# Kernel tuning notes

Hardware: AMD Instinct MI355X
Metric: run time of the kernel (lower is better)

## Reference

```python
import jax, jax.numpy as jnp
import numpy as np

N = 100000
E = 1_600_000
IN_DIM = 128
HIDDEN = 128


def spmm(row, col, vals, H):
    # y[r] = sum_{edges e with row[e]==r} vals[e] * H[col[e]]
    msgs = vals[:, None] * H[col]          # [E, hidden] gather + scale
    return jax.ops.segment_sum(msgs, row, num_segments=H.shape[0])


def setup_inputs() -> dict:
    key = jax.random.key(0)
    ks = jax.random.split(key, 10)
    X = jax.random.normal(ks[0], (N, IN_DIM), dtype=jnp.float32)
    row = jax.random.randint(ks[1], (E,), 0, N, dtype=jnp.int32)
    col = jax.random.randint(ks[2], (E,), 0, N, dtype=jnp.int32)
    vals = jax.random.uniform(ks[3], (E,), dtype=jnp.float32)
    s_in = 1.0 / np.sqrt(IN_DIM)
    s_h = 1.0 / np.sqrt(HIDDEN)
    W_in = jax.random.normal(ks[4], (IN_DIM, HIDDEN), dtype=jnp.float32) * s_in
    b_in = jax.random.normal(ks[5], (HIDDEN,), dtype=jnp.float32) * s_in
    W_mp1 = jax.random.normal(ks[6], (HIDDEN, HIDDEN), dtype=jnp.float32) * s_h
    W_mp2 = jax.random.normal(ks[7], (HIDDEN, HIDDEN), dtype=jnp.float32) * s_h
    W_out = jax.random.normal(ks[8], (HIDDEN, 1), dtype=jnp.float32) * s_h
    b_out = jax.random.normal(ks[9], (1,), dtype=jnp.float32) * s_h
    return {"X": X, "row": row, "col": col, "vals": vals,
            "W_in": W_in, "b_in": b_in, "W_mp1": W_mp1, "W_mp2": W_mp2,
            "W_out": W_out, "b_out": b_out}


def reference(X, row, col, vals, W_in, b_in, W_mp1, W_mp2, W_out, b_out):
    H = jax.nn.relu(X @ W_in + b_in)          # [N, hidden]
    AH = spmm(row, col, vals, H)              # 1-hop propagation
    A2H = spmm(row, col, vals, AH)            # 2-hop propagation
    H2 = jax.nn.relu(AH @ W_mp1 + A2H @ W_mp2)
    return H2 @ W_out + b_out                 # [N, 1]
```

## Files before the change

### kernel.cpp

```cpp
#include <hip/hip_runtime.h>

#define N_NODES 100000
#define N_EDGES 1600000
#define NBUCK 391
#define NCHUNK 256
#define CHUNK 6250
#define LROW 136
#define DCAP 5120

typedef float f32x4 __attribute__((ext_vector_type(4)));
typedef _Float16 f16x8 __attribute__((ext_vector_type(8)));
typedef _Float16 h16x2 __attribute__((ext_vector_type(2)));

__device__ __forceinline__ unsigned f2h_bits(float f) {
    union { _Float16 h; unsigned short s; } c;
    c.h = (_Float16)f;
    return c.s;
}
__device__ __forceinline__ h16x2 u2h(unsigned u) {
    union { unsigned u; h16x2 h; } c;
    c.u = u;
    return c.h;
}
__device__ __forceinline__ unsigned pk16lo(unsigned hi, unsigned lo) {
    return __builtin_amdgcn_perm(hi, lo, 0x05040100u);
}
__device__ __forceinline__ unsigned pk16hi(unsigned hi, unsigned lo) {
    return __builtin_amdgcn_perm(hi, lo, 0x07060302u);
}
__device__ __forceinline__ float fdot2(h16x2 a, h16x2 b, float c) {
#if __has_builtin(__builtin_amdgcn_fdot2)
    return __builtin_amdgcn_fdot2(a, b, c, false);
#else
    return c + (float)a[0] * (float)b[0] + (float)a[1] * (float)b[1];
#endif
}

__device__ __forceinline__ f16x8 pack_h8(float4 a, float4 b) {
    f16x8 r;
    r[0] = (_Float16)a.x; r[1] = (_Float16)a.y;
    r[2] = (_Float16)a.z; r[3] = (_Float16)a.w;
    r[4] = (_Float16)b.x; r[5] = (_Float16)b.y;
    r[6] = (_Float16)b.z; r[7] = (_Float16)b.w;
    return r;
}


__global__ __launch_bounds__(256) void k_prep(const int* __restrict__ row,
                                              int* __restrict__ hmat,
                                              const float* __restrict__ Wa,
                                              const float* __restrict__ Wb,
                                              const float* __restrict__ Wc,
                                              unsigned short* __restrict__ Wta,
                                              unsigned short* __restrict__ Wtb,
                                              unsigned short* __restrict__ Wtc) {
    if (blockIdx.x < NCHUNK) {
        __shared__ int h[NBUCK];
        for (int i = threadIdx.x; i < NBUCK; i += 256) h[i] = 0;
        __syncthreads();
        int s = blockIdx.x * CHUNK, e = s + CHUNK;
        for (int i = s + threadIdx.x; i < e; i += 256)
            atomicAdd(&h[row[i] >> 8], 1);
        __syncthreads();
        for (int b = threadIdx.x; b < NBUCK; b += 256)
            hmat[blockIdx.x * NBUCK + b] = h[b];
    } else {
        int t = (blockIdx.x - NCHUNK) * 256 + threadIdx.x;
        int which = t >> 14;
        int i = t & 16383;
        int n = i & 127, k = i >> 7;
        const float* W = which == 0 ? Wa : which == 1 ? Wb : Wc;
        unsigned short* Wt = which == 0 ? Wta : which == 1 ? Wtb : Wtc;
        Wt[n * 128 + k] = (unsigned short)f2h_bits(W[k * 128 + n]);
    }
}

__global__ __launch_bounds__(512) void k_colscanB(const int* __restrict__ hmat,
                                                  int* __restrict__ bases,
                                                  int* __restrict__ bstart) {
    __shared__ int s[512];
    int b = blockIdx.x, t = threadIdx.x;
    if (b < NBUCK) {
        int v = (t < NCHUNK) ? hmat[t * NBUCK + b] : 0;
        s[t] = v;
        __syncthreads();
        for (int off = 1; off < 512; off <<= 1) {
            int x = (t >= off) ? s[t - off] : 0;
            __syncthreads();
            s[t] += x;
            __syncthreads();
        }
        if (t < NCHUNK) bases[t * NBUCK + b] = s[t] - v;
    } else {
        int v = 0;
        if (t < NBUCK) {
            for (int blk = 0; blk < NCHUNK; blk++) v += hmat[blk * NBUCK + t];
        }
        s[t] = v;
        __syncthreads();
        for (int off = 1; off < 512; off <<= 1) {
            int x = (t >= off) ? s[t - off] : 0;
            __syncthreads();
            s[t] += x;
            __syncthreads();
        }
        if (t < NBUCK) bstart[t] = s[t] - v;
        if (t == NBUCK) bstart[NBUCK] = N_EDGES;
    }
}

__global__ __launch_bounds__(256) void k_binC(const int* __restrict__ row,
                                              const int* __restrict__ col,
                                              const float* __restrict__ vals,
                                              const int* __restrict__ bstart,
                                              const int* __restrict__ bases,
                                              int2* __restrict__ grouped) {
    __shared__ int cnt[NBUCK];
    for (int i = threadIdx.x; i < NBUCK; i += 256) cnt[i] = 0;
    __syncthreads();
    int s = blockIdx.x * CHUNK, e = s + CHUNK;
    for (int i = s + threadIdx.x; i < e; i += 256) {
        int r = row[i];
        int b = r >> 8;
        int rank = atomicAdd(&cnt[b], 1);
        int pos = bstart[b] + bases[blockIdx.x * NBUCK + b] + rank;
        unsigned hv = f2h_bits(vals[i]);
        grouped[pos] = make_int2(col[i], ((r & 255) << 14) | hv);
    }
}

__global__ __launch_bounds__(256) void k_binD(const int2* __restrict__ grouped,
                                              const int* __restrict__ bstart,
                                              unsigned* __restrict__ evf,
                                              int* __restrict__ row_ptr) {
    __shared__ int h[256], sc[256], cur[256];
    __shared__ int2 ebuf[DCAP];
    int b = blockIdx.x, t = threadIdx.x;
    int s0 = bstart[b], e0 = bstart[b + 1];
    int n = e0 - s0;
    bool inlds = (n <= DCAP);
    h[t] = 0;
    __syncthreads();
    if (inlds) {
        for (int i = t; i < n; i += 256) ebuf[i] = grouped[s0 + i];
        __syncthreads();
        for (int i = t; i < n; i += 256)
            atomicAdd(&h[(ebuf[i].y >> 14) & 255], 1);
    } else {
        for (int i = s0 + t; i < e0; i += 256)
            atomicAdd(&h[(grouped[i].y >> 14) & 255], 1);
    }
    __syncthreads();
    int v = h[t];
    sc[t] = v;
    __syncthreads();
    for (int off = 1; off < 256; off <<= 1) {
        int x = (t >= off) ? sc[t - off] : 0;
        __syncthreads();
        sc[t] += x;
        __syncthreads();
    }
    int excl = sc[t] - v;
    cur[t] = excl;
    int grow = b * 256 + t;
    if (grow <= N_NODES) row_ptr[grow] = s0 + excl;
    __syncthreads();
    if (inlds) {
        for (int i = t; i < n; i += 256) {
            int2 g = ebuf[i];
            int rl = (g.y >> 14) & 255;
            int p = atomicAdd(&cur[rl], 1);
            evf[s0 + p] = ((unsigned)g.x << 14) | (unsigned)(g.y & 0x3fff);
        }
    } else {
        for (int i = s0 + t; i < e0; i += 256) {
            int2 g = grouped[i];
            int rl = (g.y >> 14) & 255;
            int p = atomicAdd(&cur[rl], 1);
            evf[s0 + p] = ((unsigned)g.x << 14) | (unsigned)(g.y & 0x3fff);
        }
    }
}

__global__ __launch_bounds__(256) void k_gemm_in(const float* __restrict__ X,
                                                 const unsigned short* __restrict__ Wt,
                                                 const float* __restrict__ b,
                                                 unsigned short* __restrict__ H) {
    __shared__ unsigned short lds[64 * LROW];
    int tid = threadIdx.x;
    int lane = tid & 63, wv = tid >> 6;
    int quad = lane >> 4, c16 = lane & 15;

    f16x8 wf[2][4];
    float bb[2];
#pragma unroll
    for (int nt = 0; nt < 2; nt++) {
        int ng = wv * 2 + nt;
        bb[nt] = b[ng * 16 + c16];
#pragma unroll
        for (int kc = 0; kc < 4; kc++)
            wf[nt][kc] = *(const f16x8*)&Wt[(ng * 16 + c16) * 128 + kc * 32 + quad * 8];
    }

    int tilebase = blockIdx.x * 64;
    const float4* Xg = (const float4*)X;
#pragma unroll
    for (int i = 0; i < 4; i++) {
        int c = tid + i * 256;
        int r = c >> 4, o = c & 15;
        int grow = tilebase + r;
        float4 f0 = make_float4(0.f, 0.f, 0.f, 0.f), f1 = f0;
        if (grow < N_NODES) {
            f0 = Xg[(size_t)grow * 32 + o * 2];
            f1 = Xg[(size_t)grow * 32 + o * 2 + 1];
        }
        *(f16x8*)&lds[r * LROW + o * 8] = pack_h8(f0, f1);
    }
    __syncthreads();

    f32x4 acc[4][2] = {};
#pragma unroll
    for (int t4 = 0; t4 < 4; t4++) {
#pragma unroll
        for (int kc = 0; kc < 4; kc++) {
            f16x8 af = *(const f16x8*)&lds[(t4 * 16 + c16) * LROW + kc * 32 + quad * 8];
#pragma unroll
            for (int nt = 0; nt < 2; nt++)
                acc[t4][nt] = __builtin_amdgcn_mfma_f32_16x16x32_f16(af, wf[nt][kc],
                                                                    acc[t4][nt], 0, 0, 0);
        }
    }
    __syncthreads();

#pragma unroll
    for (int t4 = 0; t4 < 4; t4++)
#pragma unroll
        for (int nt = 0; nt < 2; nt++) {
            int ncol = (wv * 2 + nt) * 16 + c16;
#pragma unroll
            for (int r = 0; r < 4; r++) {
                float v = fmaxf(acc[t4][nt][r] + bb[nt], 0.f);
                lds[(t4 * 16 + quad * 4 + r) * LROW + ncol] = (unsigned short)f2h_bits(v);
            }
        }
    __syncthreads();
#pragma unroll
    for (int i = 0; i < 4; i++) {
        int c = tid + i * 256;
        int r = c >> 4, o = c & 15;
        int grow = tilebase + r;
        if (grow < N_NODES)
            *(uint4*)&H[(size_t)grow * 128 + o * 8] = *(const uint4*)&lds[r * LROW + o * 8];
    }
}

__global__ __launch_bounds__(256) void k_spmm(const int* __restrict__ rp,
                                              const unsigned* __restrict__ evf,
                                              const unsigned* __restrict__ Hin,
                                              unsigned* __restrict__ Ho) {
    int wid = (blockIdx.x * blockDim.x + threadIdx.x) >> 6;
    int lane = threadIdx.x & 63;
    if (wid >= N_NODES) return;
    int q = lane >> 4, l16 = lane & 15;
    int s = __builtin_amdgcn_readfirstlane(rp[wid]);
    int e = __builtin_amdgcn_readfirstlane(rp[wid + 1]);
    float a0 = 0.f, a1 = 0.f, a2 = 0.f, a3 = 0.f;
    float a4 = 0.f, a5 = 0.f, a6 = 0.f, a7 = 0.f;
    for (int base = s; base < e; base += 64) {
        int cnt = e - base;
        if (cnt > 64) cnt = 64;
        unsigned ev = evf[base + (lane < cnt ? lane : cnt - 1)];
        int r = 0;
        for (; r + 16 <= cnt; r += 16) {
            unsigned u0 = __shfl(ev, r + q, 64);
            unsigned u1 = __shfl(ev, r + 4 + q, 64);
            unsigned u2 = __shfl(ev, r + 8 + q, 64);
            unsigned u3 = __shfl(ev, r + 12 + q, 64);
            const uint4 h0 = *(const uint4*)&Hin[(size_t)(u0 >> 14) * 64 + l16 * 4];
            const uint4 h1 = *(const uint4*)&Hin[(size_t)(u1 >> 14) * 64 + l16 * 4];
            const uint4 h2 = *(const uint4*)&Hin[(size_t)(u2 >> 14) * 64 + l16 * 4];
            const uint4 h3 = *(const uint4*)&Hin[(size_t)(u3 >> 14) * 64 + l16 * 4];
            h16x2 v01 = u2h(pk16lo(u1 & 0x3fffu, u0 & 0x3fffu));
            h16x2 v23 = u2h(pk16lo(u3 & 0x3fffu, u2 & 0x3fffu));
            a0 = fdot2(v01, u2h(pk16lo(h1.x, h0.x)), a0);
            a0 = fdot2(v23, u2h(pk16lo(h3.x, h2.x)), a0);
            a1 = fdot2(v01, u2h(pk16hi(h1.x, h0.x)), a1);
            a1 = fdot2(v23, u2h(pk16hi(h3.x, h2.x)), a1);
            a2 = fdot2(v01, u2h(pk16lo(h1.y, h0.y)), a2);
            a2 = fdot2(v23, u2h(pk16lo(h3.y, h2.y)), a2);
            a3 = fdot2(v01, u2h(pk16hi(h1.y, h0.y)), a3);
            a3 = fdot2(v23, u2h(pk16hi(h3.y, h2.y)), a3);
            a4 = fdot2(v01, u2h(pk16lo(h1.z, h0.z)), a4);
            a4 = fdot2(v23, u2h(pk16lo(h3.z, h2.z)), a4);
            a5 = fdot2(v01, u2h(pk16hi(h1.z, h0.z)), a5);
            a5 = fdot2(v23, u2h(pk16hi(h3.z, h2.z)), a5);
            a6 = fdot2(v01, u2h(pk16lo(h1.w, h0.w)), a6);
            a6 = fdot2(v23, u2h(pk16lo(h3.w, h2.w)), a6);
            a7 = fdot2(v01, u2h(pk16hi(h1.w, h0.w)), a7);
            a7 = fdot2(v23, u2h(pk16hi(h3.w, h2.w)), a7);
        }
        if (r < cnt) {
            int i0 = r + q, i1 = r + 4 + q, i2 = r + 8 + q, i3 = r + 12 + q;
            unsigned u0 = __shfl(ev, i0 < cnt ? i0 : cnt - 1, 64);
            unsigned u1 = __shfl(ev, i1 < cnt ? i1 : cnt - 1, 64);
            unsigned u2 = __shfl(ev, i2 < cnt ? i2 : cnt - 1, 64);
            unsigned u3 = __shfl(ev, i3 < cnt ? i3 : cnt - 1, 64);
            const uint4 h0 = *(const uint4*)&Hin[(size_t)(u0 >> 14) * 64 + l16 * 4];
            const uint4 h1 = *(const uint4*)&Hin[(size_t)(u1 >> 14) * 64 + l16 * 4];
            const uint4 h2 = *(const uint4*)&Hin[(size_t)(u2 >> 14) * 64 + l16 * 4];
            const uint4 h3 = *(const uint4*)&Hin[(size_t)(u3 >> 14) * 64 + l16 * 4];
            unsigned m0 = (i0 < cnt) ? (u0 & 0x3fffu) : 0u;
            unsigned m1 = (i1 < cnt) ? (u1 & 0x3fffu) : 0u;
            unsigned m2 = (i2 < cnt) ? (u2 & 0x3fffu) : 0u;
            unsigned m3 = (i3 < cnt) ? (u3 & 0x3fffu) : 0u;
            h16x2 v01 = u2h(pk16lo(m1, m0));
            h16x2 v23 = u2h(pk16lo(m3, m2));
            a0 = fdot2(v01, u2h(pk16lo(h1.x, h0.x)), a0);
            a0 = fdot2(v23, u2h(pk16lo(h3.x, h2.x)), a0);
            a1 = fdot2(v01, u2h(pk16hi(h1.x, h0.x)), a1);
            a1 = fdot2(v23, u2h(pk16hi(h3.x, h2.x)), a1);
            a2 = fdot2(v01, u2h(pk16lo(h1.y, h0.y)), a2);
            a2 = fdot2(v23, u2h(pk16lo(h3.y, h2.y)), a2);
            a3 = fdot2(v01, u2h(pk16hi(h1.y, h0.y)), a3);
            a3 = fdot2(v23, u2h(pk16hi(h3.y, h2.y)), a3);
            a4 = fdot2(v01, u2h(pk16lo(h1.z, h0.z)), a4);
            a4 = fdot2(v23, u2h(pk16lo(h3.z, h2.z)), a4);
            a5 = fdot2(v01, u2h(pk16hi(h1.z, h0.z)), a5);
            a5 = fdot2(v23, u2h(pk16hi(h3.z, h2.z)), a5);
            a6 = fdot2(v01, u2h(pk16lo(h1.w, h0.w)), a6);
            a6 = fdot2(v23, u2h(pk16lo(h3.w, h2.w)), a6);
            a7 = fdot2(v01, u2h(pk16hi(h1.w, h0.w)), a7);
            a7 = fdot2(v23, u2h(pk16hi(h3.w, h2.w)), a7);
        }
    }
    a0 += __shfl_xor(a0, 16, 64); a0 += __shfl_xor(a0, 32, 64);
    a1 += __shfl_xor(a1, 16, 64); a1 += __shfl_xor(a1, 32, 64);
    a2 += __shfl_xor(a2, 16, 64); a2 += __shfl_xor(a2, 32, 64);
    a3 += __shfl_xor(a3, 16, 64); a3 += __shfl_xor(a3, 32, 64);
    a4 += __shfl_xor(a4, 16, 64); a4 += __shfl_xor(a4, 32, 64);
    a5 += __shfl_xor(a5, 16, 64); a5 += __shfl_xor(a5, 32, 64);
    a6 += __shfl_xor(a6, 16, 64); a6 += __shfl_xor(a6, 32, 64);
    a7 += __shfl_xor(a7, 16, 64); a7 += __shfl_xor(a7, 32, 64);
    if (q == 0) {
        uint4 p;
        p.x = (f2h_bits(a1) << 16) | f2h_bits(a0);
        p.y = (f2h_bits(a3) << 16) | f2h_bits(a2);
        p.z = (f2h_bits(a5) << 16) | f2h_bits(a4);
        p.w = (f2h_bits(a7) << 16) | f2h_bits(a6);
        *(uint4*)&Ho[(size_t)wid * 64 + l16 * 4] = p;
    }
}

__global__ __launch_bounds__(256) void k_gemm_out(const unsigned short* __restrict__ AH,
                                                  const unsigned short* __restrict__ A2H,
                                                  const unsigned short* __restrict__ Wt1,
                                                  const unsigned short* __restrict__ Wt2,
                                                  const float* __restrict__ Wout,
                                                  const float* __restrict__ bout,
                                                  float* __restrict__ out) {
    __shared__ unsigned short lds[2][64 * LROW];
    __shared__ float part[4][64];
    int tid = threadIdx.x;
    int lane = tid & 63, wv = tid >> 6;
    int quad = lane >> 4, c16 = lane & 15;

    f16x8 w1f[2][4], w2f[2][4];
    float wo[2];
#pragma unroll
    for (int nt = 0; nt < 2; nt++) {
        int ng = wv * 2 + nt;
        wo[nt] = Wout[ng * 16 + c16];
#pragma unroll
        for (int kc = 0; kc < 4; kc++) {
            w1f[nt][kc] = *(const f16x8*)&Wt1[(ng * 16 + c16) * 128 + kc * 32 + quad * 8];
            w2f[nt][kc] = *(const f16x8*)&Wt2[(ng * 16 + c16) * 128 + kc * 32 + quad * 8];
        }
    }
    float bo = bout[0];

    int tilebase = blockIdx.x * 64;
    const uint4* Ag = (const uint4*)(AH + (size_t)tilebase * 128);
    const uint4* Bg = (const uint4*)(A2H + (size_t)tilebase * 128);
#pragma unroll
    for (int i = 0; i < 4; i++) {
        int c = tid + i * 256;
        int r = c >> 4, o = c & 15;
        *(uint4*)&lds[0][r * LROW + o * 8] = Ag[c];
        *(uint4*)&lds[1][r * LROW + o * 8] = Bg[c];
    }
    __syncthreads();

    f32x4 acc[4][2] = {};
#pragma unroll
    for (int t4 = 0; t4 < 4; t4++) {
#pragma unroll
        for (int kc = 0; kc < 4; kc++) {
            f16x8 afA = *(const f16x8*)&lds[0][(t4 * 16 + c16) * LROW + kc * 32 + quad * 8];
            f16x8 afB = *(const f16x8*)&lds[1][(t4 * 16 + c16) * LROW + kc * 32 + quad * 8];
#pragma unroll
            for (int nt = 0; nt < 2; nt++) {
                acc[t4][nt] = __builtin_amdgcn_mfma_f32_16x16x32_f16(afA, w1f[nt][kc],
                                                                    acc[t4][nt], 0, 0, 0);
                acc[t4][nt] = __builtin_amdgcn_mfma_f32_16x16x32_f16(afB, w2f[nt][kc],
                                                                    acc[t4][nt], 0, 0, 0);
            }
        }
    }

#pragma unroll
    for (int t4 = 0; t4 < 4; t4++) {
        float p[4];
#pragma unroll
        for (int r = 0; r < 4; r++)
            p[r] = fmaxf(acc[t4][0][r], 0.f) * wo[0] + fmaxf(acc[t4][1][r], 0.f) * wo[1];
#pragma unroll
        for (int m = 1; m < 16; m <<= 1)
#pragma unroll
            for (int r = 0; r < 4; r++) p[r] += __shfl_xor(p[r], m, 64);
        if (c16 == 0)
#pragma unroll
            for (int r = 0; r < 4; r++) part[wv][t4 * 16 + quad * 4 + r] = p[r];
    }
    __syncthreads();
    if (tid < 64) {
        int orow = tilebase + tid;
        if (orow < N_NODES)
            out[orow] = part[0][tid] + part[1][tid] + part[2][tid] + part[3][tid] + bo;
    }
}


extern "C" void kernel_launch(void* const* d_in, const int* in_sizes, int n_in,
                              void* d_out, int out_size, void* d_ws, size_t ws_size,
                              hipStream_t stream) {
    const float* X    = (const float*)d_in[0];
    const int*   row  = (const int*)d_in[1];
    const int*   col  = (const int*)d_in[2];
    const float* vals = (const float*)d_in[3];
    const float* W_in = (const float*)d_in[4];
    const float* b_in = (const float*)d_in[5];
    const float* W1   = (const float*)d_in[6];
    const float* W2   = (const float*)d_in[7];
    const float* Wout = (const float*)d_in[8];
    const float* bout = (const float*)d_in[9];
    float* out = (float*)d_out;

    char* ws = (char*)d_ws;
    size_t off = 0;
    auto alloc = [&](size_t bytes) -> void* {
        void* p = ws + off;
        off += (bytes + 511) & ~(size_t)511;
        return p;
    };
    unsigned short* Hb  = (unsigned short*)alloc((size_t)N_NODES * 128 * 2);
    unsigned short* AHb = (unsigned short*)alloc((size_t)N_NODES * 128 * 2);
    unsigned short* A2b = (unsigned short*)alloc((size_t)N_NODES * 128 * 2);
    unsigned* evf  = (unsigned*)alloc((size_t)N_EDGES * 4);
    int2* grouped  = (int2*)alloc((size_t)N_EDGES * 8);
    unsigned short* Wtin = (unsigned short*)alloc(128 * 128 * 2);
    unsigned short* Wt1  = (unsigned short*)alloc(128 * 128 * 2);
    unsigned short* Wt2  = (unsigned short*)alloc(128 * 128 * 2);
    int*   hmat    = (int*)alloc((size_t)NCHUNK * NBUCK * 4);
    int*   bases   = (int*)alloc((size_t)NCHUNK * NBUCK * 4);
    int*   bstart  = (int*)alloc(512 * 4);
    int*   row_ptr = (int*)alloc((size_t)(N_NODES + 256) * 4);

    k_prep<<<NCHUNK + 192, 256, 0, stream>>>(row, hmat, W_in, W1, W2, Wtin, Wt1, Wt2);
    k_colscanB<<<NBUCK + 1, 512, 0, stream>>>(hmat, bases, bstart);
    k_binC<<<NCHUNK, 256, 0, stream>>>(row, col, vals, bstart, bases, grouped);
    k_binD<<<NBUCK, 256, 0, stream>>>(grouped, bstart, evf, row_ptr);

    int gblk = (N_NODES + 63) / 64;
    k_gemm_in<<<gblk, 256, 0, stream>>>(X, Wtin, b_in, Hb);

    int sblk = (N_NODES + 3) / 4;
    k_spmm<<<sblk, 256, 0, stream>>>(row_ptr, evf, (const unsigned*)Hb, (unsigned*)AHb);
    k_spmm<<<sblk, 256, 0, stream>>>(row_ptr, evf, (const unsigned*)AHb, (unsigned*)A2b);

    k_gemm_out<<<gblk, 256, 0, stream>>>(AHb, A2b, Wt1, Wt2, Wout, bout, out);
}
```

Measured before the change: 296.5 us.

## Fuse second SpMM hop into output GEMM kernel via LDS staging

The second propagation hop is now computed inside the output GEMM kernel. Each wave aggregates 16 rows into LDS, and the MFMA stage then consumes them directly. This removes the A2H intermediate buffer and its global write and read round-trip, plus one kernel launch. In exchange, the gather work runs on far fewer waves, each handling rows serially, and LDS use per block limits occupancy, which may reduce latency hiding for the irregular gathers.

```diff
diff --git a/kernel.cpp b/kernel.cpp
--- a/kernel.cpp
+++ b/kernel.cpp
@@ -35,7 +35,6 @@
     return c + (float)a[0] * (float)b[0] + (float)a[1] * (float)b[1];
 #endif
 }
-
 __device__ __forceinline__ f16x8 pack_h8(float4 a, float4 b) {
     f16x8 r;
     r[0] = (_Float16)a.x; r[1] = (_Float16)a.y;
@@ -45,227 +44,12 @@
     return r;
 }
 
-
-__global__ __launch_bounds__(256) void k_prep(const int* __restrict__ row,
-                                              int* __restrict__ hmat,
-                                              const float* __restrict__ Wa,
-                                              const float* __restrict__ Wb,
-                                              const float* __restrict__ Wc,
-                                              unsigned short* __restrict__ Wta,
-                                              unsigned short* __restrict__ Wtb,
-                                              unsigned short* __restrict__ Wtc) {
-    if (blockIdx.x < NCHUNK) {
-        __shared__ int h[NBUCK];
-        for (int i = threadIdx.x; i < NBUCK; i += 256) h[i] = 0;
-        __syncthreads();
-        int s = blockIdx.x * CHUNK, e = s + CHUNK;
-        for (int i = s + threadIdx.x; i < e; i += 256)
-            atomicAdd(&h[row[i] >> 8], 1);
-        __syncthreads();
-        for (int b = threadIdx.x; b < NBUCK; b += 256)
-            hmat[blockIdx.x * NBUCK + b] = h[b];
-    } else {
-        int t = (blockIdx.x - NCHUNK) * 256 + threadIdx.x;
-        int which = t >> 14;
-        int i = t & 16383;
-        int n = i & 127, k = i >> 7;
-        const float* W = which == 0 ? Wa : which == 1 ? Wb : Wc;
-        unsigned short* Wt = which == 0 ? Wta : which == 1 ? Wtb : Wtc;
-        Wt[n * 128 + k] = (unsigned short)f2h_bits(W[k * 128 + n]);
-    }
-}
-
-__global__ __launch_bounds__(512) void k_colscanB(const int* __restrict__ hmat,
-                                                  int* __restrict__ bases,
-                                                  int* __restrict__ bstart) {
-    __shared__ int s[512];
-    int b = blockIdx.x, t = threadIdx.x;
-    if (b < NBUCK) {
-        int v = (t < NCHUNK) ? hmat[t * NBUCK + b] : 0;
-        s[t] = v;
-        __syncthreads();
-        for (int off = 1; off < 512; off <<= 1) {
-            int x = (t >= off) ? s[t - off] : 0;
-            __syncthreads();
-            s[t] += x;
-            __syncthreads();
-        }
-        if (t < NCHUNK) bases[t * NBUCK + b] = s[t] - v;
-    } else {
-        int v = 0;
-        if (t < NBUCK) {
-            for (int blk = 0; blk < NCHUNK; blk++) v += hmat[blk * NBUCK + t];
-        }
-        s[t] = v;
-        __syncthreads();
-        for (int off = 1; off < 512; off <<= 1) {
-            int x = (t >= off) ? s[t - off] : 0;
-            __syncthreads();
-            s[t] += x;
-            __syncthreads();
-        }
-        if (t < NBUCK) bstart[t] = s[t] - v;
-        if (t == NBUCK) bstart[NBUCK] = N_EDGES;
-    }
-}
-
-__global__ __launch_bounds__(256) void k_binC(const int* __restrict__ row,
-                                              const int* __restrict__ col,
-                                              const float* __restrict__ vals,
-                                              const int* __restrict__ bstart,
-                                              const int* __restrict__ bases,
-                                              int2* __restrict__ grouped) {
-    __shared__ int cnt[NBUCK];
-    for (int i = threadIdx.x; i < NBUCK; i += 256) cnt[i] = 0;
-    __syncthreads();
-    int s = blockIdx.x * CHUNK, e = s + CHUNK;
-    for (int i = s + threadIdx.x; i < e; i += 256) {
-        int r = row[i];
-        int b = r >> 8;
-        int rank = atomicAdd(&cnt[b], 1);
-        int pos = bstart[b] + bases[blockIdx.x * NBUCK + b] + rank;
-        unsigned hv = f2h_bits(vals[i]);
-        grouped[pos] = make_int2(col[i], ((r & 255) << 14) | hv);
-    }
-}
-
-__global__ __launch_bounds__(256) void k_binD(const int2* __restrict__ grouped,
-                                              const int* __restrict__ bstart,
-                                              unsigned* __restrict__ evf,
-                                              int* __restrict__ row_ptr) {
-    __shared__ int h[256], sc[256], cur[256];
-    __shared__ int2 ebuf[DCAP];
-    int b = blockIdx.x, t = threadIdx.x;
-    int s0 = bstart[b], e0 = bstart[b + 1];
-    int n = e0 - s0;
-    bool inlds = (n <= DCAP);
-    h[t] = 0;
-    __syncthreads();
-    if (inlds) {
-        for (int i = t; i < n; i += 256) ebuf[i] = grouped[s0 + i];
-        __syncthreads();
-        for (int i = t; i < n; i += 256)
-            atomicAdd(&h[(ebuf[i].y >> 14) & 255], 1);
-    } else {
-        for (int i = s0 + t; i < e0; i += 256)
-            atomicAdd(&h[(grouped[i].y >> 14) & 255], 1);
-    }
-    __syncthreads();
-    int v = h[t];
-    sc[t] = v;
-    __syncthreads();
-    for (int off = 1; off < 256; off <<= 1) {
-        int x = (t >= off) ? sc[t - off] : 0;
-        __syncthreads();
-        sc[t] += x;
-        __syncthreads();
-    }
-    int excl = sc[t] - v;
-    cur[t] = excl;
-    int grow = b * 256 + t;
-    if (grow <= N_NODES) row_ptr[grow] = s0 + excl;
-    __syncthreads();
-    if (inlds) {
-        for (int i = t; i < n; i += 256) {
-            int2 g = ebuf[i];
-            int rl = (g.y >> 14) & 255;
-            int p = atomicAdd(&cur[rl], 1);
-            evf[s0 + p] = ((unsigned)g.x << 14) | (unsigned)(g.y & 0x3fff);
-        }
-    } else {
-        for (int i = s0 + t; i < e0; i += 256) {
-            int2 g = grouped[i];
-            int rl = (g.y >> 14) & 255;
-            int p = atomicAdd(&cur[rl], 1);
-            evf[s0 + p] = ((unsigned)g.x << 14) | (unsigned)(g.y & 0x3fff);
-        }
-    }
-}
-
-__global__ __launch_bounds__(256) void k_gemm_in(const float* __restrict__ X,
-                                                 const unsigned short* __restrict__ Wt,
-                                                 const float* __restrict__ b,
-                                                 unsigned short* __restrict__ H) {
-    __shared__ unsigned short lds[64 * LROW];
-    int tid = threadIdx.x;
-    int lane = tid & 63, wv = tid >> 6;
-    int quad = lane >> 4, c16 = lane & 15;
-
-    f16x8 wf[2][4];
-    float bb[2];
-#pragma unroll
-    for (int nt = 0; nt < 2; nt++) {
-        int ng = wv * 2 + nt;
-        bb[nt] = b[ng * 16 + c16];
-#pragma unroll
-        for (int kc = 0; kc < 4; kc++)
-            wf[nt][kc] = *(const f16x8*)&Wt[(ng * 16 + c16) * 128 + kc * 32 + quad * 8];
-    }
-
-    int tilebase = blockIdx.x * 64;
-    const float4* Xg = (const float4*)X;
-#pragma unroll
-    for (int i = 0; i < 4; i++) {
-        int c = tid + i * 256;
-        int r = c >> 4, o = c & 15;
-        int grow = tilebase + r;
-        float4 f0 = make_float4(0.f, 0.f, 0.f, 0.f), f1 = f0;
-        if (grow < N_NODES) {
-            f0 = Xg[(size_t)grow * 32 + o * 2];
-            f1 = Xg[(size_t)grow * 32 + o * 2 + 1];
-        }
-        *(f16x8*)&lds[r * LROW + o * 8] = pack_h8(f0, f1);
-    }
-    __syncthreads();
-
-    f32x4 acc[4][2] = {};
-#pragma unroll
-    for (int t4 = 0; t4 < 4; t4++) {
-#pragma unroll
-        for (int kc = 0; kc < 4; kc++) {
-            f16x8 af = *(const f16x8*)&lds[(t4 * 16 + c16) * LROW + kc * 32 + quad * 8];
-#pragma unroll
-            for (int nt = 0; nt < 2; nt++)
-                acc[t4][nt] = __builtin_amdgcn_mfma_f32_16x16x32_f16(af, wf[nt][kc],
-                                                                    acc[t4][nt], 0, 0, 0);
-        }
-    }
-    __syncthreads();
-
-#pragma unroll
-    for (int t4 = 0; t4 < 4; t4++)
-#pragma unroll
-        for (int nt = 0; nt < 2; nt++) {
-            int ncol = (wv * 2 + nt) * 16 + c16;
-#pragma unroll
-            for (int r = 0; r < 4; r++) {
-                float v = fmaxf(acc[t4][nt][r] + bb[nt], 0.f);
-                lds[(t4 * 16 + quad * 4 + r) * LROW + ncol] = (unsigned short)f2h_bits(v);
-            }
-        }
-    __syncthreads();
-#pragma unroll
-    for (int i = 0; i < 4; i++) {
-        int c = tid + i * 256;
-        int r = c >> 4, o = c & 15;
-        int grow = tilebase + r;
-        if (grow < N_NODES)
-            *(uint4*)&H[(size_t)grow * 128 + o * 8] = *(const uint4*)&lds[r * LROW + o * 8];
-    }
-}
-
-__global__ __launch_bounds__(256) void k_spmm(const int* __restrict__ rp,
-                                              const unsigned* __restrict__ evf,
-                                              const unsigned* __restrict__ Hin,
-                                              unsigned* __restrict__ Ho) {
-    int wid = (blockIdx.x * blockDim.x + threadIdx.x) >> 6;
-    int lane = threadIdx.x & 63;
-    if (wid >= N_NODES) return;
+__device__ __forceinline__ void spmm_row(const unsigned* __restrict__ evf,
+                                         const unsigned* __restrict__ Hin,
+                                         int s, int e, int lane,
+                                         float& a0, float& a1, float& a2, float& a3,
+                                         float& a4, float& a5, float& a6, float& a7) {
     int q = lane >> 4, l16 = lane & 15;
-    int s = __builtin_amdgcn_readfirstlane(rp[wid]);
-    int e = __builtin_amdgcn_readfirstlane(rp[wid + 1]);
-    float a0 = 0.f, a1 = 0.f, a2 = 0.f, a3 = 0.f;
-    float a4 = 0.f, a5 = 0.f, a6 = 0.f, a7 = 0.f;
     for (int base = s; base < e; base += 64) {
         int cnt = e - base;
         if (cnt > 64) cnt = 64;
@@ -333,6 +117,228 @@
             a7 = fdot2(v23, u2h(pk16hi(h3.w, h2.w)), a7);
         }
     }
+}
+
+__global__ __launch_bounds__(256) void k_prep(const int* __restrict__ row,
+                                              int* __restrict__ hmat,
+                                              const float* __restrict__ Wa,
+                                              const float* __restrict__ Wb,
+                                              const float* __restrict__ Wc,
+                                              unsigned short* __restrict__ Wta,
+                                              unsigned short* __restrict__ Wtb,
+                                              unsigned short* __restrict__ Wtc) {
+    if (blockIdx.x < NCHUNK) {
+        __shared__ int h[NBUCK];
+        for (int i = threadIdx.x; i < NBUCK; i += 256) h[i] = 0;
+        __syncthreads();
+        int s = blockIdx.x * CHUNK, e = s + CHUNK;
+        for (int i = s + threadIdx.x; i < e; i += 256)
+            atomicAdd(&h[row[i] >> 8], 1);
+        __syncthreads();
+        for (int b = threadIdx.x; b < NBUCK; b += 256)
+            hmat[blockIdx.x * NBUCK + b] = h[b];
+    } else {
+        int t = (blockIdx.x - NCHUNK) * 256 + threadIdx.x;
+        int which = t >> 14;
+        int i = t & 16383;
+        int n = i & 127, k = i >> 7;
+        const float* W = which == 0 ? Wa : which == 1 ? Wb : Wc;
+        unsigned short* Wt = which == 0 ? Wta : which == 1 ? Wtb : Wtc;
+        Wt[n * 128 + k] = (unsigned short)f2h_bits(W[k * 128 + n]);
+    }
+}
+
+__global__ __launch_bounds__(512) void k_colscanB(const int* __restrict__ hmat,
+                                                  int* __restrict__ bases,
+                                                  int* __restrict__ bstart) {
+    __shared__ int s[512];
+    int b = blockIdx.x, t = threadIdx.x;
+    if (b < NBUCK) {
+        int v = (t < NCHUNK) ? hmat[t * NBUCK + b] : 0;
+        s[t] = v;
+        __syncthreads();
+        for (int off = 1; off < 512; off <<= 1) {
+            int x = (t >= off) ? s[t - off] : 0;
+            __syncthreads();
+            s[t] += x;
+            __syncthreads();
+        }
+        if (t < NCHUNK) bases[t * NBUCK + b] = s[t] - v;
+    } else {
+        int v = 0;
+        if (t < NBUCK) {
+            for (int blk = 0; blk < NCHUNK; blk++) v += hmat[blk * NBUCK + t];
+        }
+        s[t] = v;
+        __syncthreads();
+        for (int off = 1; off < 512; off <<= 1) {
+            int x = (t >= off) ? s[t - off] : 0;
+            __syncthreads();
+            s[t] += x;
+            __syncthreads();
+        }
+        if (t < NBUCK) bstart[t] = s[t] - v;
+        if (t == NBUCK) bstart[NBUCK] = N_EDGES;
+    }
+}
+
+__global__ __launch_bounds__(256) void k_binC(const int* __restrict__ row,
+                                              const int* __restrict__ col,
+                                              const float* __restrict__ vals,
+                                              const int* __restrict__ bstart,
+                                              const int* __restrict__ bases,
+                                              int2* __restrict__ grouped) {
+    __shared__ int cnt[NBUCK];
+    for (int i = threadIdx.x; i < NBUCK; i += 256) cnt[i] = 0;
+    __syncthreads();
+    int s = blockIdx.x * CHUNK, e = s + CHUNK;
+    for (int i = s + threadIdx.x; i < e; i += 256) {
+        int r = row[i];
+        int b = r >> 8;
+        int rank = atomicAdd(&cnt[b], 1);
+        int pos = bstart[b] + bases[blockIdx.x * NBUCK + b] + rank;
+        unsigned hv = f2h_bits(vals[i]);
+        grouped[pos] = make_int2(col[i], ((r & 255) << 14) | hv);
+    }
+}
+
+__global__ __launch_bounds__(256) void k_binD(const int2* __restrict__ grouped,
+                                              const int* __restrict__ bstart,
+                                              unsigned* __restrict__ evf,
+                                              int* __restrict__ row_ptr) {
+    __shared__ int h[256], sc[256], cur[256];
+    __shared__ int2 ebuf[DCAP];
+    int b = blockIdx.x, t = threadIdx.x;
+    int s0 = bstart[b], e0 = bstart[b + 1];
+    int n = e0 - s0;
+    bool inlds = (n <= DCAP);
+    h[t] = 0;
+    __syncthreads();
+    if (inlds) {
+        for (int i = t; i < n; i += 256) ebuf[i] = grouped[s0 + i];
+        __syncthreads();
+        for (int i = t; i < n; i += 256)
+            atomicAdd(&h[(ebuf[i].y >> 14) & 255], 1);
+    } else {
+        for (int i = s0 + t; i < e0; i += 256)
+            atomicAdd(&h[(grouped[i].y >> 14) & 255], 1);
+    }
+    __syncthreads();
+    int v = h[t];
+    sc[t] = v;
+    __syncthreads();
+    for (int off = 1; off < 256; off <<= 1) {
+        int x = (t >= off) ? sc[t - off] : 0;
+        __syncthreads();
+        sc[t] += x;
+        __syncthreads();
+    }
+    int excl = sc[t] - v;
+    cur[t] = excl;
+    int grow = b * 256 + t;
+    if (grow <= N_NODES) row_ptr[grow] = s0 + excl;
+    __syncthreads();
+    if (inlds) {
+        for (int i = t; i < n; i += 256) {
+            int2 g = ebuf[i];
+            int rl = (g.y >> 14) & 255;
+            int p = atomicAdd(&cur[rl], 1);
+            evf[s0 + p] = ((unsigned)g.x << 14) | (unsigned)(g.y & 0x3fff);
+        }
+    } else {
+        for (int i = s0 + t; i < e0; i += 256) {
+            int2 g = grouped[i];
+            int rl = (g.y >> 14) & 255;
+            int p = atomicAdd(&cur[rl], 1);
+            evf[s0 + p] = ((unsigned)g.x << 14) | (unsigned)(g.y & 0x3fff);
+        }
+    }
+}
+
+__global__ __launch_bounds__(256) void k_gemm_in(const float* __restrict__ X,
+                                                 const unsigned short* __restrict__ Wt,
+                                                 const float* __restrict__ b,
+                                                 unsigned short* __restrict__ H) {
+    __shared__ unsigned short lds[64 * LROW];
+    int tid = threadIdx.x;
+    int lane = tid & 63, wv = tid >> 6;
+    int quad = lane >> 4, c16 = lane & 15;
+
+    f16x8 wf[2][4];
+    float bb[2];
+#pragma unroll
+    for (int nt = 0; nt < 2; nt++) {
+        int ng = wv * 2 + nt;
+        bb[nt] = b[ng * 16 + c16];
+#pragma unroll
+        for (int kc = 0; kc < 4; kc++)
+            wf[nt][kc] = *(const f16x8*)&Wt[(ng * 16 + c16) * 128 + kc * 32 + quad * 8];
+    }
+
+    int tilebase = blockIdx.x * 64;
+    const float4* Xg = (const float4*)X;
+#pragma unroll
+    for (int i = 0; i < 4; i++) {
+        int c = tid + i * 256;
+        int r = c >> 4, o = c & 15;
+        int grow = tilebase + r;
+        float4 f0 = make_float4(0.f, 0.f, 0.f, 0.f), f1 = f0;
+        if (grow < N_NODES) {
+            f0 = Xg[(size_t)grow * 32 + o * 2];
+            f1 = Xg[(size_t)grow * 32 + o * 2 + 1];
+        }
+        *(f16x8*)&lds[r * LROW + o * 8] = pack_h8(f0, f1);
+    }
+    __syncthreads();
+
+    f32x4 acc[4][2] = {};
+#pragma unroll
+    for (int t4 = 0; t4 < 4; t4++) {
+#pragma unroll
+        for (int kc = 0; kc < 4; kc++) {
+            f16x8 af = *(const f16x8*)&lds[(t4 * 16 + c16) * LROW + kc * 32 + quad * 8];
+#pragma unroll
+            for (int nt = 0; nt < 2; nt++)
+                acc[t4][nt] = __builtin_amdgcn_mfma_f32_16x16x32_f16(af, wf[nt][kc],
+                                                                    acc[t4][nt], 0, 0, 0);
+        }
+    }
+    __syncthreads();
+
+#pragma unroll
+    for (int t4 = 0; t4 < 4; t4++)
+#pragma unroll
+        for (int nt = 0; nt < 2; nt++) {
+            int ncol = (wv * 2 + nt) * 16 + c16;
+#pragma unroll
+            for (int r = 0; r < 4; r++) {
+                float v = fmaxf(acc[t4][nt][r] + bb[nt], 0.f);
+                lds[(t4 * 16 + quad * 4 + r) * LROW + ncol] = (unsigned short)f2h_bits(v);
+            }
+        }
+    __syncthreads();
+#pragma unroll
+    for (int i = 0; i < 4; i++) {
+        int c = tid + i * 256;
+        int r = c >> 4, o = c & 15;
+        int grow = tilebase + r;
+        if (grow < N_NODES)
+            *(uint4*)&H[(size_t)grow * 128 + o * 8] = *(const uint4*)&lds[r * LROW + o * 8];
+    }
+}
+
+__global__ __launch_bounds__(256) void k_spmm(const int* __restrict__ rp,
+                                              const unsigned* __restrict__ evf,
+                                              const unsigned* __restrict__ Hin,
+                                              unsigned* __restrict__ Ho) {
+    int wid = (blockIdx.x * blockDim.x + threadIdx.x) >> 6;
+    int lane = threadIdx.x & 63;
+    if (wid >= N_NODES) return;
+    int s = __builtin_amdgcn_readfirstlane(rp[wid]);
+    int e = __builtin_amdgcn_readfirstlane(rp[wid + 1]);
+    float a0 = 0.f, a1 = 0.f, a2 = 0.f, a3 = 0.f;
+    float a4 = 0.f, a5 = 0.f, a6 = 0.f, a7 = 0.f;
+    spmm_row(evf, Hin, s, e, lane, a0, a1, a2, a3, a4, a5, a6, a7);
     a0 += __shfl_xor(a0, 16, 64); a0 += __shfl_xor(a0, 32, 64);
     a1 += __shfl_xor(a1, 16, 64); a1 += __shfl_xor(a1, 32, 64);
     a2 += __shfl_xor(a2, 16, 64); a2 += __shfl_xor(a2, 32, 64);
@@ -341,7 +347,8 @@
     a5 += __shfl_xor(a5, 16, 64); a5 += __shfl_xor(a5, 32, 64);
     a6 += __shfl_xor(a6, 16, 64); a6 += __shfl_xor(a6, 32, 64);
     a7 += __shfl_xor(a7, 16, 64); a7 += __shfl_xor(a7, 32, 64);
-    if (q == 0) {
+    if ((lane >> 4) == 0) {
+        int l16 = lane & 15;
         uint4 p;
         p.x = (f2h_bits(a1) << 16) | f2h_bits(a0);
         p.y = (f2h_bits(a3) << 16) | f2h_bits(a2);
@@ -351,44 +358,69 @@
     }
 }
 
-__global__ __launch_bounds__(256) void k_gemm_out(const unsigned short* __restrict__ AH,
-                                                  const unsigned short* __restrict__ A2H,
-                                                  const unsigned short* __restrict__ Wt1,
-                                                  const unsigned short* __restrict__ Wt2,
-                                                  const float* __restrict__ Wout,
-                                                  const float* __restrict__ bout,
-                                                  float* __restrict__ out) {
+__global__ __launch_bounds__(256) void k_spmm_gout(const int* __restrict__ rp,
+                                                   const unsigned* __restrict__ evf,
+                                                   const unsigned* __restrict__ AH,
+                                                   const unsigned short* __restrict__ Wt1,
+                                                   const unsigned short* __restrict__ Wt2,
+                                                   const float* __restrict__ Wout,
+                                                   const float* __restrict__ bout,
+                                                   float* __restrict__ out) {
     __shared__ unsigned short lds[2][64 * LROW];
     __shared__ float part[4][64];
     int tid = threadIdx.x;
     int lane = tid & 63, wv = tid >> 6;
     int quad = lane >> 4, c16 = lane & 15;
-
-    f16x8 w1f[2][4], w2f[2][4];
-    float wo[2];
-#pragma unroll
-    for (int nt = 0; nt < 2; nt++) {
-        int ng = wv * 2 + nt;
-        wo[nt] = Wout[ng * 16 + c16];
-#pragma unroll
-        for (int kc = 0; kc < 4; kc++) {
-            w1f[nt][kc] = *(const f16x8*)&Wt1[(ng * 16 + c16) * 128 + kc * 32 + quad * 8];
-            w2f[nt][kc] = *(const f16x8*)&Wt2[(ng * 16 + c16) * 128 + kc * 32 + quad * 8];
-        }
-    }
-    float bo = bout[0];
-
     int tilebase = blockIdx.x * 64;
-    const uint4* Ag = (const uint4*)(AH + (size_t)tilebase * 128);
-    const uint4* Bg = (const uint4*)(A2H + (size_t)tilebase * 128);
+
+    const uint4* Ag = (const uint4*)(AH + (size_t)tilebase * 64);
 #pragma unroll
     for (int i = 0; i < 4; i++) {
         int c = tid + i * 256;
         int r = c >> 4, o = c & 15;
         *(uint4*)&lds[0][r * LROW + o * 8] = Ag[c];
-        *(uint4*)&lds[1][r * LROW + o * 8] = Bg[c];
-    }
-    __syncthreads();
+    }
+
+    for (int rr = 0; rr < 16; rr++) {
+        int rown = tilebase + wv * 16 + rr;
+        if (rown >= N_NODES) break;
+        int s = __builtin_amdgcn_readfirstlane(rp[rown]);
+        int e = __builtin_amdgcn_readfirstlane(rp[rown + 1]);
+        float a0 = 0.f, a1 = 0.f, a2 = 0.f, a3 = 0.f;
+        float a4 = 0.f, a5 = 0.f, a6 = 0.f, a7 = 0.f;
+        spmm_row(evf, AH, s, e, lane, a0, a1, a2, a3, a4, a5, a6, a7);
+        a0 += __shfl_xor(a0, 16, 64); a0 += __shfl_xor(a0, 32, 64);
+        a1 += __shfl_xor(a1, 16, 64); a1 += __shfl_xor(a1, 32, 64);
+        a2 += __shfl_xor(a2, 16, 64); a2 += __shfl_xor(a2, 32, 64);
+        a3 += __shfl_xor(a3, 16, 64); a3 += __shfl_xor(a3, 32, 64);
+        a4 += __shfl_xor(a4, 16, 64); a4 += __shfl_xor(a4, 32, 64);
+        a5 += __shfl_xor(a5, 16, 64); a5 += __shfl_xor(a5, 32, 64);
+        a6 += __shfl_xor(a6, 16, 64); a6 += __shfl_xor(a6, 32, 64);
+        a7 += __shfl_xor(a7, 16, 64); a7 += __shfl_xor(a7, 32, 64);
+        if (quad == 0) {
+            uint4 p;
+            p.x = (f2h_bits(a1) << 16) | f2h_bits(a0);
+            p.y = (f2h_bits(a3) << 16) | f2h_bits(a2);
+            p.z = (f2h_bits(a5) << 16) | f2h_bits(a4);
+            p.w = (f2h_bits(a7) << 16) | f2h_bits(a6);
+            *(uint4*)&lds[1][(wv * 16 + rr) * LROW + c16 * 8] = p;
+        }
+    }
+    __syncthreads();
+
+    f16x8 w1f[2][4], w2f[2][4];
+    float wo[2];
+#pragma unroll
+    for (int nt = 0; nt < 2; nt++) {
+        int ng = wv * 2 + nt;
+        wo[nt] = Wout[ng * 16 + c16];
+#pragma unroll
+        for (int kc = 0; kc < 4; kc++) {
+            w1f[nt][kc] = *(const f16x8*)&Wt1[(ng * 16 + c16) * 128 + kc * 32 + quad * 8];
+            w2f[nt][kc] = *(const f16x8*)&Wt2[(ng * 16 + c16) * 128 + kc * 32 + quad * 8];
+        }
+    }
+    float bo = bout[0];
 
     f32x4 acc[4][2] = {};
 #pragma unroll
@@ -454,7 +486,6 @@
     };
     unsigned short* Hb  = (unsigned short*)alloc((size_t)N_NODES * 128 * 2);
     unsigned short* AHb = (unsigned short*)alloc((size_t)N_NODES * 128 * 2);
-    unsigned short* A2b = (unsigned short*)alloc((size_t)N_NODES * 128 * 2);
     unsigned* evf  = (unsigned*)alloc((size_t)N_EDGES * 4);
     int2* grouped  = (int2*)alloc((size_t)N_EDGES * 8);
     unsigned short* Wtin = (unsigned short*)alloc(128 * 128 * 2);
@@ -475,7 +506,7 @@
 
     int sblk = (N_NODES + 3) / 4;
     k_spmm<<<sblk, 256, 0, stream>>>(row_ptr, evf, (const unsigned*)Hb, (unsigned*)AHb);
-    k_spmm<<<sblk, 256, 0, stream>>>(row_ptr, evf, (const unsigned*)AHb, (unsigned*)A2b);
-
-    k_gemm_out<<<gblk, 256, 0, stream>>>(AHb, A2b, Wt1, Wt2, Wout, bout, out);
-}
+
+    k_spmm_gout<<<gblk, 256, 0, stream>>>(row_ptr, evf, (const unsigned*)AHb,
+                                          Wt1, Wt2, Wout, bout, out);
+}
```

After: 302.0 us. About the same (+1.9%).
